# Optimization experiments

Hardware: AMD Instinct MI355X
Metric: run time of the kernel (lower is better)

The kernel has to match this reference:

```python
import jax, jax.numpy as jnp
import numpy as np

N_NODES = 50000
N_EDGES = 800000
N_GRAPHS = 128
D = 128
L = 4
C = 10
GN_EPS = 1e-5


def setup_inputs() -> dict:
    key = jax.random.key(0)
    ks = jax.random.split(key, 12)
    s = 0.05
    x = jax.random.normal(ks[0], (N_NODES, D), dtype=jnp.float32)
    gin_w1 = jax.random.normal(ks[1], (L, D, D), dtype=jnp.float32) * s
    gin_b1 = jax.random.normal(ks[2], (L, D), dtype=jnp.float32) * s
    gin_w2 = jax.random.normal(ks[3], (L, D, D), dtype=jnp.float32) * s
    gin_b2 = jax.random.normal(ks[4], (L, D), dtype=jnp.float32) * s
    gn_weight = jnp.ones((L, D), dtype=jnp.float32)
    gn_bias = jnp.zeros((L, D), dtype=jnp.float32)
    gn_scale = jnp.ones((L, D), dtype=jnp.float32)
    fw1 = jax.random.normal(ks[5], (D, D), dtype=jnp.float32) * s
    fb1 = jnp.zeros((D,), dtype=jnp.float32)
    fw2 = jax.random.normal(ks[6], (D, D), dtype=jnp.float32) * s
    fb2 = jnp.zeros((D,), dtype=jnp.float32)
    fw3 = jax.random.normal(ks[7], (D, C), dtype=jnp.float32) * s
    fb3 = jnp.zeros((C,), dtype=jnp.float32)
    edge_index = jax.random.randint(ks[8], (2, N_EDGES), 0, N_NODES, dtype=jnp.int64)
    batch = jnp.sort(jax.random.randint(ks[9], (N_NODES,), 0, N_GRAPHS, dtype=jnp.int64))
    return dict(x=x, gin_w1=gin_w1, gin_b1=gin_b1, gin_w2=gin_w2, gin_b2=gin_b2,
                gn_weight=gn_weight, gn_bias=gn_bias, gn_scale=gn_scale,
                fw1=fw1, fb1=fb1, fw2=fw2, fb2=fb2, fw3=fw3, fb3=fb3,
                edge_index=edge_index, batch=batch)


def _graph_norm(h, batch, weight, bias, mean_scale, counts):
    # PyG GraphNorm: per-graph mean/var with learnable mean_scale.
    mean = jax.ops.segment_sum(h, batch, num_segments=N_GRAPHS) / counts  # [G, D]
    out = h - mean[batch] * mean_scale
    var = jax.ops.segment_sum(out * out, batch, num_segments=N_GRAPHS) / counts
    return weight * out / jnp.sqrt(var[batch] + GN_EPS) + bias


def reference(x, gin_w1, gin_b1, gin_w2, gin_b2, gn_weight, gn_bias, gn_scale,
              fw1, fb1, fw2, fb2, fw3, fb3, edge_index, batch):
    src, dst = edge_index[0], edge_index[1]
    ones = jnp.ones((N_NODES, 1), dtype=x.dtype)
    counts = jnp.maximum(jax.ops.segment_sum(ones, batch, num_segments=N_GRAPHS), 1.0)  # [G,1]
    h = x
    for l in range(L):
        # GINConv, eps=0: (1+eps)*x + sum_{j->i} x_j, then MLP with act after each Linear
        agg = jax.ops.segment_sum(h[src], dst, num_segments=N_NODES)  # [N, D]
        h = h + agg
        h = jax.nn.relu(h @ gin_w1[l] + gin_b1[l])
        h = jax.nn.relu(h @ gin_w2[l] + gin_b2[l])
        h = _graph_norm(h, batch, gn_weight[l], gn_bias[l], gn_scale[l], counts)
        h = jax.nn.relu(h)
    # sum readout per graph
    g = jax.ops.segment_sum(h, batch, num_segments=N_GRAPHS)  # [G, D]
    # final MLP (dropout is identity in eval)
    g = jax.nn.relu(g @ fw1 + fb1)
    g = jax.nn.relu(g @ fw2 + fb2)
    out = g @ fw3 + fb3
    return jax.nn.log_softmax(out, axis=-1)
```

## Files before the change

kernel.cpp:

```cpp
#include <hip/hip_runtime.h>
#include <cstddef>

#define N_NODES 50000
#define N_EDGES 800000
#define N_GRAPHS 128
#define DIM 128
#define N_LAYERS 4
#define GN_EPS 1e-5f

#define B_CHUNK 256
#define EPB 3125
#define BUCKET_SHIFT 9
#define BUCKET_SIZE 512
#define NB 98

#define CX_BLKS 12500
#define CW_BLKS 512
#define GB_BLKS 196
#define SETUP_BLKS (CX_BLKS + CW_BLKS + GB_BLKS + B_CHUNK)

typedef unsigned short ushort_t;
typedef __attribute__((ext_vector_type(8))) short frag8;
typedef __attribute__((ext_vector_type(4))) float f32x4;

__device__ inline float bfbits2f(unsigned hi16) { return __uint_as_float(hi16 << 16); }
__device__ inline ushort_t bf16rne(float v) {
    unsigned u = __float_as_uint(v);
    unsigned r = u + 0x7fff + ((u >> 16) & 1);
    return (ushort_t)(r >> 16);
}
__device__ inline unsigned packbf2(float a, float b) {
    return (unsigned)bf16rne(a) | ((unsigned)bf16rne(b) << 16);
}
__device__ inline void bf16split(float v, ushort_t& h, ushort_t& l) {
    ushort_t hi = bf16rne(v);
    float fh = __uint_as_float(((unsigned)hi) << 16);
    l = bf16rne(v - fh);
    h = hi;
}

__global__ __launch_bounds__(256) void setup_misc(const float* __restrict__ x, unsigned* __restrict__ Hb,
                                                  const float* __restrict__ w1, const float* __restrict__ w2,
                                                  ushort_t* __restrict__ whi, ushort_t* __restrict__ wlo,
                                                  const int* __restrict__ batch, int* __restrict__ gstart,
                                                  const int* __restrict__ edst, int* __restrict__ cnts) {
    __shared__ int cnt[NB];
    int b = blockIdx.x, t = threadIdx.x;
    if (b < CX_BLKS) {
        int i = b * 256 + t;
        if (i < N_NODES * 64) {
            float a = x[2 * i], bb = x[2 * i + 1];
            Hb[i] = packbf2(a, bb);
        }
    } else if (b < CX_BLKS + CW_BLKS) {
        int idx = (b - CX_BLKS) * 256 + t;
        int mat = idx >> 14;
        int e = idx & 16383;
        int n = e >> 7, k = e & 127;
        int l = mat >> 1;
        const float* src = (mat & 1) ? (w2 + (size_t)l * DIM * DIM) : (w1 + (size_t)l * DIM * DIM);
        float v = src[k * DIM + n];
        ushort_t h, lw;
        bf16split(v, h, lw);
        whi[(size_t)mat * DIM * DIM + n * DIM + k] = h;
        wlo[(size_t)mat * DIM * DIM + n * DIM + k] = lw;
    } else if (b < CX_BLKS + CW_BLKS + GB_BLKS) {
        int i = (b - CX_BLKS - CW_BLKS) * 256 + t;
        if (i < N_NODES) {
            int bb = batch[i];
            if (i == 0) {
                for (int g = 0; g <= bb; ++g) gstart[g] = 0;
            } else {
                int pb = batch[i - 1];
                for (int g = pb + 1; g <= bb; ++g) gstart[g] = i;
            }
            if (i == N_NODES - 1) {
                for (int g = bb + 1; g <= N_GRAPHS; ++g) gstart[g] = N_NODES;
            }
        }
    } else {
        int blk = b - (CX_BLKS + CW_BLKS + GB_BLKS);
        for (int i = t; i < NB; i += 256) cnt[i] = 0;
        __syncthreads();
        int base = blk * EPB;
        for (int i = t; i < EPB; i += 256) atomicAdd(&cnt[edst[base + i] >> BUCKET_SHIFT], 1);
        __syncthreads();
        for (int i = t; i < NB; i += 256) cnts[i * B_CHUNK + blk] = cnt[i];
    }
}

__global__ __launch_bounds__(1024) void scan_local(const int* __restrict__ in, int* __restrict__ out,
                                                   int* __restrict__ bsum, int n) {
    __shared__ int wsum[16];
    int tid = threadIdx.x, lane = tid & 63, w = tid >> 6;
    int gi = blockIdx.x * 1024 + tid;
    int v = (gi < n) ? in[gi] : 0;
    int s = v;
    #pragma unroll
    for (int off = 1; off < 64; off <<= 1) {
        int t = __shfl_up(s, off, 64);
        if (lane >= off) s += t;
    }
    if (lane == 63) wsum[w] = s;
    __syncthreads();
    if (w == 0) {
        int ws = (lane < 16) ? wsum[lane] : 0;
        #pragma unroll
        for (int off = 1; off < 16; off <<= 1) {
            int t = __shfl_up(ws, off, 64);
            if (lane >= off) ws += t;
        }
        if (lane < 16) wsum[lane] = ws;
    }
    __syncthreads();
    int woff = (w > 0) ? wsum[w - 1] : 0;
    if (gi < n) out[gi] = woff + s - v;
    if (tid == 1023) bsum[blockIdx.x] = woff + s;
}

__global__ __launch_bounds__(1024) void scan_add(int* __restrict__ out, const int* __restrict__ bsum,
                                                 int n, int total) {
    int lane = threadIdx.x & 63;
    int v = (lane < (int)blockIdx.x) ? bsum[lane] : 0;
    #pragma unroll
    for (int off = 1; off < 64; off <<= 1) v += __shfl_xor(v, off, 64);
    int gi = blockIdx.x * 1024 + threadIdx.x;
    if (gi < n) out[gi] += v;
    if (blockIdx.x == 0 && threadIdx.x == 0) out[n] = total;
}

__global__ __launch_bounds__(256) void p3_place(const int* __restrict__ src, const int* __restrict__ dst,
                                                const int* __restrict__ off, unsigned* __restrict__ ebuf) {
    __shared__ int cur[NB];
    int t = threadIdx.x, blk = blockIdx.x;
    for (int i = t; i < NB; i += 256) cur[i] = off[i * B_CHUNK + blk];
    __syncthreads();
    int base = blk * EPB;
    for (int i = t; i < EPB; i += 256) {
        int d = dst[base + i];
        int b = d >> BUCKET_SHIFT;
        int pos = atomicAdd(&cur[b], 1);
        ebuf[pos] = (unsigned)src[base + i] | ((unsigned)(d & (BUCKET_SIZE - 1)) << 16);
    }
}

__global__ __launch_bounds__(512) void p4_csr(const unsigned* __restrict__ ebuf, const int* __restrict__ off,
                                              int* __restrict__ eoff, int* __restrict__ csr) {
    __shared__ int cnt[BUCKET_SIZE];
    __shared__ int wsum[8];
    int k = blockIdx.x, t = threadIdx.x;
    int bstart = off[k * B_CHUNK];
    int bend = off[(k + 1) * B_CHUNK];
    cnt[t] = 0;
    __syncthreads();
    for (int i = bstart + t; i < bend; i += 512) atomicAdd(&cnt[ebuf[i] >> 16], 1);
    __syncthreads();
    int lane = t & 63, w = t >> 6;
    int v = cnt[t], s = v;
    #pragma unroll
    for (int o = 1; o < 64; o <<= 1) {
        int tt = __shfl_up(s, o, 64);
        if (lane >= o) s += tt;
    }
    if (lane == 63) wsum[w] = s;
    __syncthreads();
    if (w == 0) {
        int ws = (lane < 8) ? wsum[lane] : 0;
        #pragma unroll
        for (int o = 1; o < 8; o <<= 1) {
            int tt = __shfl_up(ws, o, 64);
            if (lane >= o) ws += tt;
        }
        if (lane < 8) wsum[lane] = ws;
    }
    __syncthreads();
    int woff = (w > 0) ? wsum[w - 1] : 0;
    int excl = woff + s - v;
    int node = k * BUCKET_SIZE + t;
    if (node < N_NODES) eoff[node] = bstart + excl;
    __syncthreads();
    cnt[t] = excl;
    __syncthreads();
    for (int i = bstart + t; i < bend; i += 512) {
        unsigned p = ebuf[i];
        int pos = atomicAdd(&cnt[p >> 16], 1);
        csr[bstart + pos] = (int)(p & 0xffffu);
    }
    if (k == NB - 1 && t == 0) eoff[N_NODES] = N_EDGES;
}

__global__ __launch_bounds__(256) void agg_bf16(const uint4* __restrict__ h4, const int* __restrict__ eoff,
                                                const int* __restrict__ csr, uint4* __restrict__ T4) {
    int wid = (blockIdx.x * 256 + threadIdx.x) >> 6;
    int lane = threadIdx.x & 63;
    int qtr = lane >> 4;
    int ql = lane & 15;
    if (wid >= N_NODES) return;
    int lo = eoff[wid], hi = eoff[wid + 1];

    float a[8];
    #pragma unroll
    for (int k = 0; k < 8; ++k) a[k] = 0.f;

    auto acc_row = [&](uint4 w) {
        a[0] += bfbits2f(w.x & 0xffffu); a[1] += bfbits2f(w.x >> 16);
        a[2] += bfbits2f(w.y & 0xffffu); a[3] += bfbits2f(w.y >> 16);
        a[4] += bfbits2f(w.z & 0xffffu); a[5] += bfbits2f(w.z >> 16);
        a[6] += bfbits2f(w.w & 0xffffu); a[7] += bfbits2f(w.w >> 16);
    };

    if (qtr == 0) acc_row(h4[(size_t)wid * 16 + ql]);

    for (int base = lo; base < hi; base += 64) {
        int nav = hi - base;
        if (nav > 64) nav = 64;
        int jv = (base + lane < hi) ? csr[base + lane] : 0;
        int cmin = nav >> 2;
        int cmax = (nav + 3) >> 2;
        int i = 0;
        for (; i + 3 < cmin; i += 4) {
            int j0 = __shfl(jv, 4 * (i + 0) + qtr, 64);
            int j1 = __shfl(jv, 4 * (i + 1) + qtr, 64);
            int j2 = __shfl(jv, 4 * (i + 2) + qtr, 64);
            int j3 = __shfl(jv, 4 * (i + 3) + qtr, 64);
            uint4 w0 = h4[(size_t)j0 * 16 + ql];
            uint4 w1 = h4[(size_t)j1 * 16 + ql];
            uint4 w2 = h4[(size_t)j2 * 16 + ql];
            uint4 w3 = h4[(size_t)j3 * 16 + ql];
            acc_row(w0); acc_row(w1); acc_row(w2); acc_row(w3);
        }
        for (; i < cmin; ++i) {
            int j = __shfl(jv, 4 * i + qtr, 64);
            acc_row(h4[(size_t)j * 16 + ql]);
        }
        for (; i < cmax; ++i) {
            int epos = 4 * i + qtr;
            int j = __shfl(jv, epos, 64);
            if (epos < nav) acc_row(h4[(size_t)j * 16 + ql]);
        }
    }

    #pragma unroll
    for (int k = 0; k < 8; ++k) {
        a[k] += __shfl_down(a[k], 32, 64);
        a[k] += __shfl_down(a[k], 16, 64);
    }
    if (qtr == 0) {
        uint4 o;
        o.x = packbf2(a[0], a[1]);
        o.y = packbf2(a[2], a[3]);
        o.z = packbf2(a[4], a[5]);
        o.w = packbf2(a[6], a[7]);
        T4[(size_t)wid * 16 + ql] = o;
    }
}

__global__ __launch_bounds__(512) void mm_layer(const ushort_t* __restrict__ A,
                                                const ushort_t* __restrict__ W1h, const ushort_t* __restrict__ W1l,
                                                const ushort_t* __restrict__ W2h, const ushort_t* __restrict__ W2l,
                                                const float* __restrict__ b1, const float* __restrict__ b2,
                                                ushort_t* __restrict__ Zb) {
    __shared__ ushort_t As[256 * 128];
    __shared__ ushort_t Ws[128 * 128];
    int tid = threadIdx.x;
    int row0 = blockIdx.x * 256;
    int wave = tid >> 6, lane = tid & 63;
    int q = lane >> 4, mn = lane & 15;

    f32x4 acc[2][8];
    #pragma unroll
    for (int t = 0; t < 2; ++t)
        #pragma unroll
        for (int n = 0; n < 8; ++n) acc[t][n] = (f32x4)(0.f);

    #pragma unroll
    for (int i = 0; i < 8; ++i) {
        int c = tid + i * 512;
        int r = c >> 4, c8 = c & 15;
        uint4 v = make_uint4(0u, 0u, 0u, 0u);
        int gr = row0 + r;
        if (gr < N_NODES) v = *(const uint4*)(A + (size_t)gr * DIM + c8 * 8);
        *(uint4*)(&As[r * 128 + (c8 ^ (r & 7)) * 8]) = v;
    }
    auto stageW = [&](const ushort_t* src) {
        #pragma unroll
        for (int i = 0; i < 4; ++i) {
            int c = tid + i * 512;
            int r = c >> 4, c8 = c & 15;
            uint4 v = *(const uint4*)(src + r * DIM + c8 * 8);
            *(uint4*)(&Ws[r * 128 + (c8 ^ (r & 7)) * 8]) = v;
        }
    };
    auto compute = [&]() {
        #pragma unroll
        for (int ks = 0; ks < 4; ++ks) {
            int m0 = wave * 32 + mn;
            int m1 = m0 + 16;
            frag8 a0 = *(const frag8*)&As[m0 * 128 + (((ks * 4 + q) ^ (m0 & 7)) * 8)];
            frag8 a1 = *(const frag8*)&As[m1 * 128 + (((ks * 4 + q) ^ (m1 & 7)) * 8)];
            #pragma unroll
            for (int n = 0; n < 8; ++n) {
                int nr = n * 16 + mn;
                frag8 b = *(const frag8*)&Ws[nr * 128 + (((ks * 4 + q) ^ (nr & 7)) * 8)];
                acc[0][n] = __builtin_amdgcn_mfma_f32_16x16x32_bf16(a0, b, acc[0][n], 0, 0, 0);
                acc[1][n] = __builtin_amdgcn_mfma_f32_16x16x32_bf16(a1, b, acc[1][n], 0, 0, 0);
            }
        }
    };

    stageW(W1h);
    __syncthreads(); compute(); __syncthreads();
    stageW(W1l);
    __syncthreads(); compute(); __syncthreads();

    int mloc = wave * 32;
    #pragma unroll
    for (int t = 0; t < 2; ++t) {
        #pragma unroll
        for (int n = 0; n < 8; ++n) {
            int col = n * 16 + mn;
            float bv = b1[col];
            #pragma unroll
            for (int r = 0; r < 4; ++r) {
                int rloc = mloc + t * 16 + q * 4 + r;
                float v = fmaxf(acc[t][n][r] + bv, 0.f);
                As[rloc * 128 + ((col >> 3) ^ (rloc & 7)) * 8 + (col & 7)] = bf16rne(v);
                acc[t][n][r] = 0.f;
            }
        }
    }
    __syncthreads();
    stageW(W2h);
    __syncthreads(); compute(); __syncthreads();
    stageW(W2l);
    __syncthreads(); compute();

    #pragma unroll
    for (int t = 0; t < 2; ++t) {
        #pragma unroll
        for (int n = 0; n < 8; ++n) {
            int col = n * 16 + mn;
            float bv = b2[col];
            #pragma unroll
            for (int r = 0; r < 4; ++r) {
                int grow = row0 + mloc + t * 16 + q * 4 + r;
                if (grow < N_NODES)
                    Zb[(size_t)grow * DIM + col] = bf16rne(fmaxf(acc[t][n][r] + bv, 0.f));
            }
        }
    }
}

__global__ __launch_bounds__(1024) void gn_fused(const unsigned* __restrict__ Zb, const int* __restrict__ gstart,
                                                 const float* __restrict__ scale, const float* __restrict__ weight,
                                                 const float* __restrict__ bias,
                                                 unsigned* __restrict__ Hb) {
    __shared__ float2 sh1[1024], sh2[1024];
    __shared__ float sa[64], sb[64];
    int g = blockIdx.x >> 1, half = blockIdx.x & 1;
    int dpl = threadIdx.x & 31, rg = threadIdx.x >> 5;
    int dp = half * 32 + dpl;
    int s = gstart[g], e = gstart[g + 1];
    float2 s1 = make_float2(0.f, 0.f), s2 = make_float2(0.f, 0.f);
    for (int n = s + rg; n < e; n += 32) {
        unsigned zz = Zb[(size_t)n * 64 + dp];
        float z0 = bfbits2f(zz & 0xffffu), z1 = bfbits2f(zz >> 16);
        s1.x += z0; s1.y += z1;
        s2.x += z0 * z0; s2.y += z1 * z1;
    }
    sh1[threadIdx.x] = s1;
    sh2[threadIdx.x] = s2;
    __syncthreads();
    if (rg == 0) {
        #pragma unroll
        for (int k = 1; k < 32; ++k) {
            float2 t1 = sh1[dpl + 32 * k], t2 = sh2[dpl + 32 * k];
            s1.x += t1.x; s1.y += t1.y;
            s2.x += t2.x; s2.y += t2.y;
        }
        int cnt = e - s;
        float cf = (float)(cnt > 0 ? cnt : 1);
        int d0 = dp * 2, d1 = d0 + 1;
        float m0 = s1.x / cf, m1 = s1.y / cf;
        float ez0 = s2.x / cf, ez1 = s2.y / cf;
        float sc0 = scale[d0], sc1 = scale[d1];
        float var0 = fmaxf(ez0 - (2.0f - sc0) * sc0 * m0 * m0, 0.f);
        float var1 = fmaxf(ez1 - (2.0f - sc1) * sc1 * m1 * m1, 0.f);
        sa[dpl * 2] = m0 * sc0;
        sa[dpl * 2 + 1] = m1 * sc1;
        sb[dpl * 2] = weight[d0] / sqrtf(var0 + GN_EPS);
        sb[dpl * 2 + 1] = weight[d1] / sqrtf(var1 + GN_EPS);
    }
    __syncthreads();
    float as0 = sa[dpl * 2], bm0 = sb[dpl * 2], bi0 = bias[dp * 2];
    float as1 = sa[dpl * 2 + 1], bm1 = sb[dpl * 2 + 1], bi1 = bias[dp * 2 + 1];
    for (int n = s + rg; n < e; n += 32) {
        unsigned zz = Zb[(size_t)n * 64 + dp];
        float z0 = bfbits2f(zz & 0xffffu), z1 = bfbits2f(zz >> 16);
        float o0 = fmaxf((z0 - as0) * bm0 + bi0, 0.f);
        float o1 = fmaxf((z1 - as1) * bm1 + bi1, 0.f);
        Hb[(size_t)n * 64 + dp] = packbf2(o0, o1);
    }
}

__global__ __launch_bounds__(1024) void gn_last(const unsigned* __restrict__ Zb, const int* __restrict__ gstart,
                                                const float* __restrict__ scale, const float* __restrict__ weight,
                                                const float* __restrict__ bias,
                                                const float* __restrict__ fw1, const float* __restrict__ fb1,
                                                const float* __restrict__ fw2, const float* __restrict__ fb2,
                                                const float* __restrict__ fw3, const float* __restrict__ fb3,
                                                float* __restrict__ out) {
    __shared__ float2 sh1[1024], sh2[1024];
    __shared__ float sa[128], sb[128];
    __shared__ float v0[128], v1[128], v2[128], lg[10];
    int g = blockIdx.x;
    int t = threadIdx.x;
    int dp = t & 63, rg = t >> 6;
    int s = gstart[g], e = gstart[g + 1];
    float2 s1 = make_float2(0.f, 0.f), s2 = make_float2(0.f, 0.f);
    for (int n = s + rg; n < e; n += 16) {
        unsigned zz = Zb[(size_t)n * 64 + dp];
        float z0 = bfbits2f(zz & 0xffffu), z1 = bfbits2f(zz >> 16);
        s1.x += z0; s1.y += z1;
        s2.x += z0 * z0; s2.y += z1 * z1;
    }
    sh1[t] = s1;
    sh2[t] = s2;
    __syncthreads();
    if (rg == 0) {
        #pragma unroll
        for (int k = 1; k < 16; ++k) {
            float2 t1 = sh1[dp + 64 * k], t2 = sh2[dp + 64 * k];
            s1.x += t1.x; s1.y += t1.y;
            s2.x += t2.x; s2.y += t2.y;
        }
        int cnt = e - s;
        float cf = (float)(cnt > 0 ? cnt : 1);
        int d0 = dp * 2, d1 = d0 + 1;
        float m0 = s1.x / cf, m1 = s1.y / cf;
        float ez0 = s2.x / cf, ez1 = s2.y / cf;
        float sc0 = scale[d0], sc1 = scale[d1];
        float var0 = fmaxf(ez0 - (2.0f - sc0) * sc0 * m0 * m0, 0.f);
        float var1 = fmaxf(ez1 - (2.0f - sc1) * sc1 * m1 * m1, 0.f);
        sa[d0] = m0 * sc0;
        sa[d1] = m1 * sc1;
        sb[d0] = weight[d0] / sqrtf(var0 + GN_EPS);
        sb[d1] = weight[d1] / sqrtf(var1 + GN_EPS);
    }
    __syncthreads();
    int d0 = dp * 2, d1 = d0 + 1;
    float as0 = sa[d0], bm0 = sb[d0], bi0 = bias[d0];
    float as1 = sa[d1], bm1 = sb[d1], bi1 = bias[d1];
    float2 rsum = make_float2(0.f, 0.f);
    for (int n = s + rg; n < e; n += 16) {
        unsigned zz = Zb[(size_t)n * 64 + dp];
        float z0 = bfbits2f(zz & 0xffffu), z1 = bfbits2f(zz >> 16);
        rsum.x += fmaxf((z0 - as0) * bm0 + bi0, 0.f);
        rsum.y += fmaxf((z1 - as1) * bm1 + bi1, 0.f);
    }
    __syncthreads();
    sh1[t] = rsum;
    __syncthreads();
    if (rg == 0) {
        #pragma unroll
        for (int k = 1; k < 16; ++k) {
            float2 t1 = sh1[dp + 64 * k];
            rsum.x += t1.x; rsum.y += t1.y;
        }
        v0[d0] = rsum.x;
        v0[d1] = rsum.y;
    }
    __syncthreads();
    if (t < 128) {
        float acc = fb1[t];
        for (int d = 0; d < 128; ++d) acc += v0[d] * fw1[d * 128 + t];
        v1[t] = fmaxf(acc, 0.f);
    }
    __syncthreads();
    if (t < 128) {
        float acc = fb2[t];
        for (int d = 0; d < 128; ++d) acc += v1[d] * fw2[d * 128 + t];
        v2[t] = fmaxf(acc, 0.f);
    }
    __syncthreads();
    if (t < 10) {
        float acc = fb3[t];
        for (int d = 0; d < 128; ++d) acc += v2[d] * fw3[d * 10 + t];
        lg[t] = acc;
    }
    __syncthreads();
    if (t < 10) {
        float m = -1e30f;
        for (int c = 0; c < 10; ++c) m = fmaxf(m, lg[c]);
        float ssum = 0.f;
        for (int c = 0; c < 10; ++c) ssum += expf(lg[c] - m);
        out[g * 10 + t] = lg[t] - m - logf(ssum);
    }
}

extern "C" void kernel_launch(void* const* d_in, const int* in_sizes, int n_in,
                              void* d_out, int out_size, void* d_ws, size_t ws_size,
                              hipStream_t stream) {
    const float* x      = (const float*)d_in[0];
    const float* gin_w1 = (const float*)d_in[1];
    const float* gin_b1 = (const float*)d_in[2];
    const float* gin_w2 = (const float*)d_in[3];
    const float* gin_b2 = (const float*)d_in[4];
    const float* gn_w   = (const float*)d_in[5];
    const float* gn_b   = (const float*)d_in[6];
    const float* gn_s   = (const float*)d_in[7];
    const float* fw1    = (const float*)d_in[8];
    const float* fb1    = (const float*)d_in[9];
    const float* fw2    = (const float*)d_in[10];
    const float* fb2    = (const float*)d_in[11];
    const float* fw3    = (const float*)d_in[12];
    const float* fb3    = (const float*)d_in[13];
    const int*   eidx   = (const int*)d_in[14];
    const int*   batch  = (const int*)d_in[15];
    float* out = (float*)d_out;

    const int* esrc = eidx;
    const int* edst = eidx + N_EDGES;

    auto align_up = [](size_t v) { return (v + 255) & ~(size_t)255; };
    char* p = (char*)d_ws;
    unsigned* Hb = (unsigned*)p;   p += align_up((size_t)N_NODES * DIM * 2);
    unsigned* Tb = (unsigned*)p;   p += align_up((size_t)N_NODES * DIM * 2);
    unsigned* Zb = (unsigned*)p;   p += align_up((size_t)N_NODES * DIM * 2);
    ushort_t* WThi = (ushort_t*)p; p += align_up((size_t)8 * DIM * DIM * 2);
    ushort_t* WTlo = (ushort_t*)p; p += align_up((size_t)8 * DIM * DIM * 2);
    int* gstart = (int*)p;         p += align_up((N_GRAPHS + 1) * 4);
    int* cnts = (int*)p;           p += align_up((size_t)NB * B_CHUNK * 4);
    int* off = (int*)p;            p += align_up(((size_t)NB * B_CHUNK + 1) * 4);
    int* bsum = (int*)p;           p += align_up(64 * 4);
    unsigned* ebuf = (unsigned*)p; p += align_up((size_t)N_EDGES * 4);
    int* eoff = (int*)p;           p += align_up((N_NODES + 1) * 4);
    int* csr = (int*)p;            p += align_up((size_t)N_EDGES * 4);

    const int SCAN_N = NB * B_CHUNK;
    const int SCAN_BLKS = (SCAN_N + 1023) / 1024;
    setup_misc<<<SETUP_BLKS, 256, 0, stream>>>(x, Hb, gin_w1, gin_w2, WThi, WTlo,
                                               batch, gstart, edst, cnts);
    scan_local<<<SCAN_BLKS, 1024, 0, stream>>>(cnts, off, bsum, SCAN_N);
    scan_add<<<SCAN_BLKS, 1024, 0, stream>>>(off, bsum, SCAN_N, N_EDGES);
    p3_place<<<B_CHUNK, 256, 0, stream>>>(esrc, edst, off, ebuf);
    p4_csr<<<NB, 512, 0, stream>>>(ebuf, off, eoff, csr);

    const int mm_grid = (N_NODES + 255) / 256;
    for (int l = 0; l < N_LAYERS; ++l) {
        agg_bf16<<<(N_NODES + 3) / 4, 256, 0, stream>>>((const uint4*)Hb, eoff, csr, (uint4*)Tb);
        mm_layer<<<mm_grid, 512, 0, stream>>>((const ushort_t*)Tb,
            WThi + (size_t)(2 * l) * DIM * DIM, WTlo + (size_t)(2 * l) * DIM * DIM,
            WThi + (size_t)(2 * l + 1) * DIM * DIM, WTlo + (size_t)(2 * l + 1) * DIM * DIM,
            gin_b1 + l * DIM, gin_b2 + l * DIM, (ushort_t*)Zb);
        if (l == N_LAYERS - 1)
            gn_last<<<N_GRAPHS, 1024, 0, stream>>>(Zb, gstart, gn_s + l * DIM,
                gn_w + l * DIM, gn_b + l * DIM, fw1, fb1, fw2, fb2, fw3, fb3, out);
        else
            gn_fused<<<N_GRAPHS * 2, 1024, 0, stream>>>(Zb, gstart, gn_s + l * DIM,
                gn_w + l * DIM, gn_b + l * DIM, Hb);
    }
}
```

Baseline: 384.9 us.

## Fuse neighbor aggregation into the per-layer MFMA MLP kernel

Removes the separate aggregation kernel and gathers neighbor sums directly into the shared-memory A tile inside mm_layer, with each wave aggregating 32 rows. This drops the intermediate T buffer's global write and read and one launch per layer. In exchange, the gather now runs on only about 196 blocks of 8 waves, so far fewer waves are available to hide random-access latency than with the old 12500-block launch.

After: 548.2 us. +42.4%, slower.

```diff
diff --git a/kernel.cpp b/kernel.cpp
--- a/kernel.cpp
+++ b/kernel.cpp
@@ -189,73 +189,8 @@
     if (k == NB - 1 && t == 0) eoff[N_NODES] = N_EDGES;
 }
 
-__global__ __launch_bounds__(256) void agg_bf16(const uint4* __restrict__ h4, const int* __restrict__ eoff,
-                                                const int* __restrict__ csr, uint4* __restrict__ T4) {
-    int wid = (blockIdx.x * 256 + threadIdx.x) >> 6;
-    int lane = threadIdx.x & 63;
-    int qtr = lane >> 4;
-    int ql = lane & 15;
-    if (wid >= N_NODES) return;
-    int lo = eoff[wid], hi = eoff[wid + 1];
-
-    float a[8];
-    #pragma unroll
-    for (int k = 0; k < 8; ++k) a[k] = 0.f;
-
-    auto acc_row = [&](uint4 w) {
-        a[0] += bfbits2f(w.x & 0xffffu); a[1] += bfbits2f(w.x >> 16);
-        a[2] += bfbits2f(w.y & 0xffffu); a[3] += bfbits2f(w.y >> 16);
-        a[4] += bfbits2f(w.z & 0xffffu); a[5] += bfbits2f(w.z >> 16);
-        a[6] += bfbits2f(w.w & 0xffffu); a[7] += bfbits2f(w.w >> 16);
-    };
-
-    if (qtr == 0) acc_row(h4[(size_t)wid * 16 + ql]);
-
-    for (int base = lo; base < hi; base += 64) {
-        int nav = hi - base;
-        if (nav > 64) nav = 64;
-        int jv = (base + lane < hi) ? csr[base + lane] : 0;
-        int cmin = nav >> 2;
-        int cmax = (nav + 3) >> 2;
-        int i = 0;
-        for (; i + 3 < cmin; i += 4) {
-            int j0 = __shfl(jv, 4 * (i + 0) + qtr, 64);
-            int j1 = __shfl(jv, 4 * (i + 1) + qtr, 64);
-            int j2 = __shfl(jv, 4 * (i + 2) + qtr, 64);
-            int j3 = __shfl(jv, 4 * (i + 3) + qtr, 64);
-            uint4 w0 = h4[(size_t)j0 * 16 + ql];
-            uint4 w1 = h4[(size_t)j1 * 16 + ql];
-            uint4 w2 = h4[(size_t)j2 * 16 + ql];
-            uint4 w3 = h4[(size_t)j3 * 16 + ql];
-            acc_row(w0); acc_row(w1); acc_row(w2); acc_row(w3);
-        }
-        for (; i < cmin; ++i) {
-            int j = __shfl(jv, 4 * i + qtr, 64);
-            acc_row(h4[(size_t)j * 16 + ql]);
-        }
-        for (; i < cmax; ++i) {
-            int epos = 4 * i + qtr;
-            int j = __shfl(jv, epos, 64);
-            if (epos < nav) acc_row(h4[(size_t)j * 16 + ql]);
-        }
-    }
-
-    #pragma unroll
-    for (int k = 0; k < 8; ++k) {
-        a[k] += __shfl_down(a[k], 32, 64);
-        a[k] += __shfl_down(a[k], 16, 64);
-    }
-    if (qtr == 0) {
-        uint4 o;
-        o.x = packbf2(a[0], a[1]);
-        o.y = packbf2(a[2], a[3]);
-        o.z = packbf2(a[4], a[5]);
-        o.w = packbf2(a[6], a[7]);
-        T4[(size_t)wid * 16 + ql] = o;
-    }
-}
-
-__global__ __launch_bounds__(512) void mm_layer(const ushort_t* __restrict__ A,
+__global__ __launch_bounds__(512) void mm_layer(const uint4* __restrict__ h4,
+                                                const int* __restrict__ eoff, const int* __restrict__ csr,
                                                 const ushort_t* __restrict__ W1h, const ushort_t* __restrict__ W1l,
                                                 const ushort_t* __restrict__ W2h, const ushort_t* __restrict__ W2l,
                                                 const float* __restrict__ b1, const float* __restrict__ b2,
@@ -266,22 +201,8 @@
     int row0 = blockIdx.x * 256;
     int wave = tid >> 6, lane = tid & 63;
     int q = lane >> 4, mn = lane & 15;
-
-    f32x4 acc[2][8];
-    #pragma unroll
-    for (int t = 0; t < 2; ++t)
-        #pragma unroll
-        for (int n = 0; n < 8; ++n) acc[t][n] = (f32x4)(0.f);
-
-    #pragma unroll
-    for (int i = 0; i < 8; ++i) {
-        int c = tid + i * 512;
-        int r = c >> 4, c8 = c & 15;
-        uint4 v = make_uint4(0u, 0u, 0u, 0u);
-        int gr = row0 + r;
-        if (gr < N_NODES) v = *(const uint4*)(A + (size_t)gr * DIM + c8 * 8);
-        *(uint4*)(&As[r * 128 + (c8 ^ (r & 7)) * 8]) = v;
-    }
+    int qtr = lane >> 4, ql = lane & 15;
+
     auto stageW = [&](const ushort_t* src) {
         #pragma unroll
         for (int i = 0; i < 4; ++i) {
@@ -291,6 +212,76 @@
             *(uint4*)(&Ws[r * 128 + (c8 ^ (r & 7)) * 8]) = v;
         }
     };
+
+    stageW(W1h);
+
+    for (int rr = 0; rr < 32; ++rr) {
+        int rloc = wave * 32 + rr;
+        int node = row0 + rloc;
+        float a[8];
+        #pragma unroll
+        for (int k = 0; k < 8; ++k) a[k] = 0.f;
+
+        auto acc_row = [&](uint4 w) {
+            a[0] += bfbits2f(w.x & 0xffffu); a[1] += bfbits2f(w.x >> 16);
+            a[2] += bfbits2f(w.y & 0xffffu); a[3] += bfbits2f(w.y >> 16);
+            a[4] += bfbits2f(w.z & 0xffffu); a[5] += bfbits2f(w.z >> 16);
+            a[6] += bfbits2f(w.w & 0xffffu); a[7] += bfbits2f(w.w >> 16);
+        };
+
+        if (node < N_NODES) {
+            int lo = eoff[node], hi = eoff[node + 1];
+            if (qtr == 0) acc_row(h4[(size_t)node * 16 + ql]);
+            for (int base = lo; base < hi; base += 64) {
+                int nav = hi - base;
+                if (nav > 64) nav = 64;
+                int jv = (base + lane < hi) ? csr[base + lane] : 0;
+                int cmin = nav >> 2;
+                int cmax = (nav + 3) >> 2;
+                int i = 0;
+                for (; i + 3 < cmin; i += 4) {
+                    int j0 = __shfl(jv, 4 * (i + 0) + qtr, 64);
+                    int j1 = __shfl(jv, 4 * (i + 1) + qtr, 64);
+                    int j2 = __shfl(jv, 4 * (i + 2) + qtr, 64);
+                    int j3 = __shfl(jv, 4 * (i + 3) + qtr, 64);
+                    uint4 w0 = h4[(size_t)j0 * 16 + ql];
+                    uint4 w1 = h4[(size_t)j1 * 16 + ql];
+                    uint4 w2 = h4[(size_t)j2 * 16 + ql];
+                    uint4 w3 = h4[(size_t)j3 * 16 + ql];
+                    acc_row(w0); acc_row(w1); acc_row(w2); acc_row(w3);
+                }
+                for (; i < cmin; ++i) {
+                    int j = __shfl(jv, 4 * i + qtr, 64);
+                    acc_row(h4[(size_t)j * 16 + ql]);
+                }
+                for (; i < cmax; ++i) {
+                    int epos = 4 * i + qtr;
+                    int j = __shfl(jv, epos, 64);
+                    if (epos < nav) acc_row(h4[(size_t)j * 16 + ql]);
+                }
+            }
+        }
+        #pragma unroll
+        for (int k = 0; k < 8; ++k) {
+            a[k] += __shfl_down(a[k], 32, 64);
+            a[k] += __shfl_down(a[k], 16, 64);
+        }
+        if (qtr == 0) {
+            uint4 o;
+            o.x = packbf2(a[0], a[1]);
+            o.y = packbf2(a[2], a[3]);
+            o.z = packbf2(a[4], a[5]);
+            o.w = packbf2(a[6], a[7]);
+            *(uint4*)(&As[rloc * 128 + ((ql ^ (rloc & 7)) * 8)]) = o;
+        }
+    }
+
+    f32x4 acc[2][8];
+    #pragma unroll
+    for (int t = 0; t < 2; ++t)
+        #pragma unroll
+        for (int n = 0; n < 8; ++n) acc[t][n] = (f32x4)(0.f);
+
     auto compute = [&]() {
         #pragma unroll
         for (int ks = 0; ks < 4; ++ks) {
@@ -308,7 +299,6 @@
         }
     };
 
-    stageW(W1h);
     __syncthreads(); compute(); __syncthreads();
     stageW(W1l);
     __syncthreads(); compute(); __syncthreads();
@@ -525,7 +515,6 @@
     auto align_up = [](size_t v) { return (v + 255) & ~(size_t)255; };
     char* p = (char*)d_ws;
     unsigned* Hb = (unsigned*)p;   p += align_up((size_t)N_NODES * DIM * 2);
-    unsigned* Tb = (unsigned*)p;   p += align_up((size_t)N_NODES * DIM * 2);
     unsigned* Zb = (unsigned*)p;   p += align_up((size_t)N_NODES * DIM * 2);
     ushort_t* WThi = (ushort_t*)p; p += align_up((size_t)8 * DIM * DIM * 2);
     ushort_t* WTlo = (ushort_t*)p; p += align_up((size_t)8 * DIM * DIM * 2);
@@ -548,8 +537,7 @@
 
     const int mm_grid = (N_NODES + 255) / 256;
     for (int l = 0; l < N_LAYERS; ++l) {
-        agg_bf16<<<(N_NODES + 3) / 4, 256, 0, stream>>>((const uint4*)Hb, eoff, csr, (uint4*)Tb);
-        mm_layer<<<mm_grid, 512, 0, stream>>>((const ushort_t*)Tb,
+        mm_layer<<<mm_grid, 512, 0, stream>>>((const uint4*)Hb, eoff, csr,
             WThi + (size_t)(2 * l) * DIM * DIM, WTlo + (size_t)(2 * l) * DIM * DIM,
             WThi + (size_t)(2 * l + 1) * DIM * DIM, WTlo + (size_t)(2 * l + 1) * DIM * DIM,
             gin_b1 + l * DIM, gin_b2 + l * DIM, (ushort_t*)Zb);
```
